# Optimization experiments

Measured on AMD Instinct MI355X. Metric: run time of the kernel, lower is better.

The kernel has to match this reference:

```python
import jax, jax.numpy as jnp
import numpy as np

HEADS = 8
DIM_HEADS = 64
M_DIM = 512
X_DIM = 512
MEM_NUM = 512
N = 16384
PERCENT = 0.25
LAY_NUMBER = 2       # outer refinement iterations
CROSS_LAYERS = 2     # layers inside M_cross_layers
EPS = 1e-5


def setup_inputs() -> dict:
    key = jax.random.key(0)
    ks = jax.random.split(key, 8)
    data = jax.random.normal(ks[0], (N, X_DIM), dtype=jnp.float32)
    Memory = jax.random.normal(ks[1], (MEM_NUM, M_DIM), dtype=jnp.float32)
    # to_kv: Linear(X_dim, 2*kv_dim, bias=False); kv_dim = heads*dim_heads
    Wkv = jax.random.normal(ks[2], (X_DIM, 2 * HEADS * DIM_HEADS), dtype=jnp.float32) * 0.02
    # per cross layer: to_q (no bias) and mutl_heads (with bias)
    Wq = jax.random.normal(ks[3], (CROSS_LAYERS, M_DIM, HEADS * DIM_HEADS), dtype=jnp.float32) * 0.02
    Wm = jax.random.normal(ks[4], (CROSS_LAYERS, HEADS * DIM_HEADS, M_DIM), dtype=jnp.float32) * 0.02
    bm = jnp.zeros((CROSS_LAYERS, M_DIM), dtype=jnp.float32)
    return {"data": data, "Memory": Memory, "Wkv": Wkv, "Wq": Wq, "Wm": Wm, "bm": bm, "istest": 0}


def _layer_norm(x):
    # F.layer_norm over last dim, no affine params
    mu = jnp.mean(x, axis=-1, keepdims=True)
    var = jnp.var(x, axis=-1, keepdims=True)
    return (x - mu) * jax.lax.rsqrt(var + EPS)


def _cross_layer(M, X, Wkv, Wq_l, Wm_l, bm_l):
    # cross_att + residual + layernorm (SublayerConnection); FFN is dead code in source
    q = (M @ Wq_l).reshape(MEM_NUM, HEADS, DIM_HEADS).transpose(1, 0, 2)      # [h, m, dh]
    kv = X @ Wkv                                                              # [n, 2*h*dh]
    k, v = jnp.split(kv, 2, axis=-1)
    k = k.reshape(-1, HEADS, DIM_HEADS).transpose(1, 0, 2)                    # [h, n, dh]
    v = v.reshape(-1, HEADS, DIM_HEADS).transpose(1, 0, 2)
    sim = jnp.einsum('hid,hjd->hij', q, k) * (DIM_HEADS ** -0.5)              # [h, m, n]
    att = jax.nn.softmax(sim, axis=-1)
    o = jnp.einsum('hij,hjd->hid', att, v)                                    # [h, m, dh]
    o = o.transpose(1, 0, 2).reshape(MEM_NUM, HEADS * DIM_HEADS)
    out = o @ Wm_l + bm_l                                                     # [m, M_dim]
    return _layer_norm(out + M)


def _cross_layers(M, X, Wkv, Wq, Wm, bm):
    for l in range(CROSS_LAYERS):
        M = _cross_layer(M, X, Wkv, Wq[l], Wm[l], bm[l])
    return M


def _calucate_sim(data, M):
    # per-sample landmark similarity: max scaled dot product against memory rows
    logits = (data @ M.T) * (DIM_HEADS ** -0.5)   # [N, mem]
    return jnp.max(logits, axis=-1)               # [N]


def _calucate_emb(data, M):
    logits = (data @ M.T) * (DIM_HEADS ** -0.5)   # [N, mem]
    logp = jax.nn.log_softmax(logits, axis=-1)
    p = jnp.exp(logp)
    out_ebs = p @ M                               # soft memory readout [N, M_dim]
    result_loss = -jnp.mean(jnp.max(logp, axis=-1))
    lse = jax.scipy.special.logsumexp(logits, axis=-1)
    zloss = jnp.mean(lse ** 2)                    # router-style z-loss
    return out_ebs, result_loss, zloss


def _select(data, sim_M, k):
    _, top_idx = jax.lax.top_k(sim_M, k)
    X = jnp.zeros_like(data)
    return X.at[top_idx].set(data[top_idx])


def reference(data, Memory, Wkv, Wq, Wm, bm, istest):
    M = Memory
    sim_M = _calucate_sim(data, M)
    percent_count = int(data.shape[0] * PERCENT)
    if not istest:
        X = _select(data, sim_M, percent_count)
        for _ in range(LAY_NUMBER):
            M = _cross_layers(M, X, Wkv, Wq, Wm, bm)
            sim_M = _calucate_sim(data, M)
            X = _select(data, sim_M, percent_count)
    out_ebs, result_loss, zloss = _calucate_emb(data, M)
    return (sim_M, out_ebs, result_loss, zloss)
```

## Files before the change

### kernel.cpp

```cpp
#include <hip/hip_runtime.h>
#include <cstdint>

#define N_DATA 16384
#define DIM 512
#define MEM 512
#define KSEL 4096
#define NH 8
#define DH 64
#define KVDIM 1024
#define SCALE 0.125f
#define ZCNT 12288.0f
#define LN_EPS 1e-5f
#define NSPLIT 4

typedef unsigned short u16;
using short8 = __attribute__((ext_vector_type(8))) short;
using f32x4  = __attribute__((ext_vector_type(4))) float;

__device__ __forceinline__ unsigned fenc(float x) {
    unsigned u = __float_as_uint(x);
    return (u & 0x80000000u) ? ~u : (u | 0x80000000u);
}
__device__ __forceinline__ u16 f2bf(float x) {
    unsigned u = __float_as_uint(x);
    u += 0x7fffu + ((u >> 16) & 1u);
    return (u16)(u >> 16);
}
__device__ __forceinline__ float bf2f(u16 h) { return __uint_as_float(((unsigned)h) << 16); }

__device__ __forceinline__ float waveSum(float v) {
#pragma unroll
    for (int o = 32; o > 0; o >>= 1) v += __shfl_down(v, o, 64);
    return v;
}
__device__ float blockSum(float v) {
    __shared__ float sh[4];
    __syncthreads();
    v = waveSum(v);
    if ((threadIdx.x & 63) == 0) sh[threadIdx.x >> 6] = v;
    __syncthreads();
    if (threadIdx.x == 0) { float s = sh[0]; for (int i = 1; i < 4; ++i) s += sh[i]; sh[0] = s; }
    __syncthreads();
    return sh[0];
}

template<int ROWS, int NW, bool GATHER>
__device__ __forceinline__ void stage_tile(const u16* __restrict__ src, int ld, int k0,
                                           int row0, const int* __restrict__ gidx,
                                           u16* lds, int wave)
{
    constexpr int NI = ROWS / 16;
    const int lane = threadIdx.x & 63;
#pragma unroll
    for (int i = wave; i < NI; i += NW) {
        const int ch = i * 64 + lane;
        const int r = ch >> 2, cc = ch & 3;
        int rg = row0 + r;
        if (GATHER) rg = gidx[rg];
        const u16* g = src + (long)rg * ld + k0 + cc * 8;
        u16* l = lds + i * 512;
        __builtin_amdgcn_global_load_lds((const __attribute__((address_space(1))) void*)g,
                                         (__attribute__((address_space(3))) void*)l,
                                         16, 0, 0);
    }
}

template<int WM, int WN, bool GATHER, int EPI, bool BIAS>
__global__ __launch_bounds__(WM * WN * 64)
void mfma_gemm(const u16* __restrict__ A, const u16* __restrict__ B,
               const float* __restrict__ bias, const int* __restrict__ gidx,
               void* __restrict__ Cv, unsigned* __restrict__ simenc,
               int K, int lda, int ldb, int ldc,
               long zsA, long zsB, long zsC, int zdiv, long zsplitC, float alpha)
{
    constexpr int BM = WM * 64, BN = WN * 64, NW = WM * WN;
    __shared__ __align__(16) u16 As[BM * 32];
    __shared__ __align__(16) u16 Bs[BN * 32];

    const int t = threadIdx.x;
    const int wave = t >> 6, lane = t & 63;
    const int wr = wave / WN, wc = wave % WN;
    const int l15 = lane & 15, l4 = lane >> 4;
    const int bm0 = blockIdx.x * BM, bn0 = blockIdx.y * BN;
    const int zs = (int)blockIdx.z % zdiv;
    const int zh = (int)blockIdx.z / zdiv;
    A += (long)zh * zsA;
    B += (long)zh * zsB;

    f32x4 acc[4][4];
#pragma unroll
    for (int i = 0; i < 4; ++i)
#pragma unroll
        for (int j = 0; j < 4; ++j)
#pragma unroll
            for (int r = 0; r < 4; ++r) acc[i][j][r] = 0.f;

    const int Kd = K / zdiv;
    const int kbeg = zs * Kd;
    for (int k0 = kbeg; k0 < kbeg + Kd; k0 += 32) {
        stage_tile<BM, NW, GATHER>(A, lda, k0, bm0, gidx, As, wave);
        stage_tile<BN, NW, false>(B, ldb, k0, bn0, nullptr, Bs, wave);
        __syncthreads();
        short8 a[4], b[4];
#pragma unroll
        for (int fm = 0; fm < 4; ++fm)
            a[fm] = *(const short8*)(As + (wr * 64 + fm * 16 + l15) * 32 + l4 * 8);
#pragma unroll
        for (int fn = 0; fn < 4; ++fn)
            b[fn] = *(const short8*)(Bs + (wc * 64 + fn * 16 + l15) * 32 + l4 * 8);
#pragma unroll
        for (int fm = 0; fm < 4; ++fm)
#pragma unroll
            for (int fn = 0; fn < 4; ++fn)
                acc[fm][fn] = __builtin_amdgcn_mfma_f32_16x16x32_bf16(a[fm], b[fn], acc[fm][fn], 0, 0, 0);
        __syncthreads();
    }

    if (EPI == 0) {
        float* C = (float*)Cv + (long)zh * zsC + (long)zs * zsplitC;
#pragma unroll
        for (int fm = 0; fm < 4; ++fm)
#pragma unroll
            for (int fn = 0; fn < 4; ++fn)
#pragma unroll
                for (int r = 0; r < 4; ++r) {
                    const int row = bm0 + wr * 64 + fm * 16 + l4 * 4 + r;
                    const int col = bn0 + wc * 64 + fn * 16 + l15;
                    float v = alpha * acc[fm][fn][r];
                    if (BIAS) v += bias[col];
                    C[(long)row * ldc + col] = v;
                }
    } else {
        u16* C = (u16*)Cv + (long)zh * zsC + (long)zs * zsplitC;
#pragma unroll
        for (int fm = 0; fm < 4; ++fm)
#pragma unroll
            for (int fn = 0; fn < 4; ++fn)
#pragma unroll
                for (int r = 0; r < 4; ++r) {
                    const int row = bm0 + wr * 64 + fm * 16 + l4 * 4 + r;
                    const int col = bn0 + wc * 64 + fn * 16 + l15;
                    float v = alpha * acc[fm][fn][r];
                    if (BIAS) v += bias[col];
                    C[(long)row * ldc + col] = f2bf(v);
                }
    }
    (void)simenc;
}

template<int EPI>
__global__ __launch_bounds__(512)
void mfma_gemm_row(const u16* __restrict__ A, const u16* __restrict__ B,
                   const float* __restrict__ bias, const float* __restrict__ Min,
                   unsigned* __restrict__ simenc,
                   float* __restrict__ Mout, u16* __restrict__ Obf,
                   float* __restrict__ simf, float* __restrict__ lse,
                   float* __restrict__ mlp, float alpha)
{
    __shared__ __align__(16) u16 As[64 * 32];
    __shared__ __align__(16) u16 Bs[512 * 32];
    const int t = threadIdx.x, wave = t >> 6, lane = t & 63;
    const int wc = wave;
    const int l15 = lane & 15, l4 = lane >> 4;
    const int bm0 = blockIdx.x * 64;

    f32x4 acc[4][4];
#pragma unroll
    for (int i = 0; i < 4; ++i)
#pragma unroll
        for (int j = 0; j < 4; ++j)
#pragma unroll
            for (int r = 0; r < 4; ++r) acc[i][j][r] = 0.f;

    for (int k0 = 0; k0 < 512; k0 += 32) {
        stage_tile<64, 8, false>(A, 512, k0, bm0, nullptr, As, wave);
        stage_tile<512, 8, false>(B, 512, k0, 0, nullptr, Bs, wave);
        __syncthreads();
        short8 a[4], b[4];
#pragma unroll
        for (int fm = 0; fm < 4; ++fm)
            a[fm] = *(const short8*)(As + (fm * 16 + l15) * 32 + l4 * 8);
#pragma unroll
        for (int fn = 0; fn < 4; ++fn)
            b[fn] = *(const short8*)(Bs + (wc * 64 + fn * 16 + l15) * 32 + l4 * 8);
#pragma unroll
        for (int fm = 0; fm < 4; ++fm)
#pragma unroll
            for (int fn = 0; fn < 4; ++fn)
                acc[fm][fn] = __builtin_amdgcn_mfma_f32_16x16x32_bf16(a[fm], b[fn], acc[fm][fn], 0, 0, 0);
        __syncthreads();
    }

    float* red  = (float*)As;
    float* red2 = red + 512;
    float* rowv = (float*)Bs;

    if (EPI == 0) {
#pragma unroll
        for (int fm = 0; fm < 4; ++fm)
#pragma unroll
            for (int r = 0; r < 4; ++r) {
                float mx = alpha * acc[fm][0][r];
#pragma unroll
                for (int fn = 1; fn < 4; ++fn) mx = fmaxf(mx, alpha * acc[fm][fn][r]);
#pragma unroll
                for (int o = 1; o <= 8; o <<= 1) mx = fmaxf(mx, __shfl_xor(mx, o, 64));
                if (l15 == 0) red[(fm * 16 + l4 * 4 + r) * 8 + wc] = mx;
            }
        __syncthreads();
        if (t < 64) {
            float mx = red[t * 8];
#pragma unroll
            for (int j = 1; j < 8; ++j) mx = fmaxf(mx, red[t * 8 + j]);
            simenc[bm0 + t] = fenc(mx);
        }
    } else if (EPI == 1) {
        float v[4][4][4];
#pragma unroll
        for (int fm = 0; fm < 4; ++fm)
#pragma unroll
            for (int fn = 0; fn < 4; ++fn) {
                const int col = wc * 64 + fn * 16 + l15;
                const float bi = bias[col];
#pragma unroll
                for (int r = 0; r < 4; ++r) {
                    const int row = bm0 + fm * 16 + l4 * 4 + r;
                    v[fm][fn][r] = acc[fm][fn][r] + bi + Min[(long)row * 512 + col];
                }
            }
#pragma unroll
        for (int fm = 0; fm < 4; ++fm)
#pragma unroll
            for (int r = 0; r < 4; ++r) {
                float s = 0.f, s2 = 0.f;
#pragma unroll
                for (int fn = 0; fn < 4; ++fn) { const float x = v[fm][fn][r]; s += x; s2 += x * x; }
#pragma unroll
                for (int o = 1; o <= 8; o <<= 1) { s += __shfl_xor(s, o, 64); s2 += __shfl_xor(s2, o, 64); }
                if (l15 == 0) {
                    red [(fm * 16 + l4 * 4 + r) * 8 + wc] = s;
                    red2[(fm * 16 + l4 * 4 + r) * 8 + wc] = s2;
                }
            }
        __syncthreads();
        if (t < 64) {
            float s = 0.f, s2 = 0.f;
#pragma unroll
            for (int j = 0; j < 8; ++j) { s += red[t * 8 + j]; s2 += red2[t * 8 + j]; }
            const float mu = s * (1.f / 512.f);
            const float var = s2 * (1.f / 512.f) - mu * mu;
            rowv[t] = mu;
            rowv[64 + t] = rsqrtf(var + LN_EPS);
        }
        __syncthreads();
#pragma unroll
        for (int fm = 0; fm < 4; ++fm)
#pragma unroll
            for (int r = 0; r < 4; ++r) {
                const int rl = fm * 16 + l4 * 4 + r;
                const float mu = rowv[rl], rs = rowv[64 + rl];
#pragma unroll
                for (int fn = 0; fn < 4; ++fn) {
                    const int col = wc * 64 + fn * 16 + l15;
                    const float y = (v[fm][fn][r] - mu) * rs;
                    Mout[(long)(bm0 + rl) * 512 + col] = y;
                    Obf [(long)(bm0 + rl) * 512 + col] = f2bf(y);
                }
            }
    } else {
#pragma unroll
        for (int fm = 0; fm < 4; ++fm)
#pragma unroll
            for (int r = 0; r < 4; ++r) {
                float mx = alpha * acc[fm][0][r];
#pragma unroll
                for (int fn = 1; fn < 4; ++fn) mx = fmaxf(mx, alpha * acc[fm][fn][r]);
#pragma unroll
                for (int o = 1; o <= 8; o <<= 1) mx = fmaxf(mx, __shfl_xor(mx, o, 64));
                if (l15 == 0) red[(fm * 16 + l4 * 4 + r) * 8 + wc] = mx;
            }
        __syncthreads();
        if (t < 64) {
            float mx = red[t * 8];
#pragma unroll
            for (int j = 1; j < 8; ++j) mx = fmaxf(mx, red[t * 8 + j]);
            rowv[t] = mx;
        }
        __syncthreads();
#pragma unroll
        for (int fm = 0; fm < 4; ++fm)
#pragma unroll
            for (int r = 0; r < 4; ++r) {
                const int rl = fm * 16 + l4 * 4 + r;
                const float m = rowv[rl];
                float s = 0.f;
#pragma unroll
                for (int fn = 0; fn < 4; ++fn) s += __expf(alpha * acc[fm][fn][r] - m);
#pragma unroll
                for (int o = 1; o <= 8; o <<= 1) s += __shfl_xor(s, o, 64);
                if (l15 == 0) red[rl * 8 + wc] = s;
            }
        __syncthreads();
        if (t < 64) {
            float s = 0.f;
#pragma unroll
            for (int j = 0; j < 8; ++j) s += red[t * 8 + j];
            const float m = rowv[t];
            const float l = m + __logf(s);
            const int gr = bm0 + t;
            simf[gr] = m; lse[gr] = l; mlp[gr] = m - l;
            rowv[64 + t] = l;
        }
        __syncthreads();
#pragma unroll
        for (int fm = 0; fm < 4; ++fm)
#pragma unroll
            for (int r = 0; r < 4; ++r) {
                const int rl = fm * 16 + l4 * 4 + r;
                const float l = rowv[64 + rl];
#pragma unroll
                for (int fn = 0; fn < 4; ++fn) {
                    const int col = wc * 64 + fn * 16 + l15;
                    Obf[(long)(bm0 + rl) * 512 + col] = f2bf(__expf(alpha * acc[fm][fn][r] - l));
                }
            }
    }
}

__global__ __launch_bounds__(256)
void flash_att(const u16* __restrict__ Q, const u16* __restrict__ KV,
               const u16* __restrict__ VT,
               float* __restrict__ oPart, float* __restrict__ mPart,
               float* __restrict__ lPart)
{
    __shared__ __align__(16) u16 Qs[64 * 64];
    __shared__ __align__(16) u16 Ks[2][64 * 64];
    __shared__ __align__(16) u16 Vs[2][64 * 64];
    __shared__ __align__(16) u16 Ps[4][16 * 72];

    const int qt = blockIdx.x, h = blockIdx.y, sp = blockIdx.z;
    const int t = threadIdx.x, wave = t >> 6, lane = t & 63;
    const int l15 = lane & 15, l4 = lane >> 4;

    const u16* Qg = Q + (long)(qt * 64) * 512 + h * 64;
    const u16* Kg = KV + ((long)sp * 1024) * 1024 + h * 64;
    const u16* Vg = VT + ((long)h * 64) * 4096 + sp * 1024;

    auto stageKV = [&](int kt, int buf) {
        const u16* Kt = Kg + (long)(kt * 64) * 1024;
        const u16* Vt = Vg + kt * 64;
#pragma unroll
        for (int i = wave; i < 8; i += 4) {
            const int ch = i * 64 + lane, r = ch >> 3, s = ch & 7;
            __builtin_amdgcn_global_load_lds(
                (const __attribute__((address_space(1))) void*)(Kt + (long)r * 1024 + ((s ^ (r & 7)) * 8)),
                (__attribute__((address_space(3))) void*)(Ks[buf] + i * 512), 16, 0, 0);
        }
#pragma unroll
        for (int i = wave; i < 8; i += 4) {
            const int ch = i * 64 + lane, r = ch >> 3, s = ch & 7;
            __builtin_amdgcn_global_load_lds(
                (const __attribute__((address_space(1))) void*)(Vt + (long)r * 4096 + ((s ^ (r & 7)) * 8)),
                (__attribute__((address_space(3))) void*)(Vs[buf] + i * 512), 16, 0, 0);
        }
    };

#pragma unroll
    for (int i = wave; i < 8; i += 4) {
        const int ch = i * 64 + lane, r = ch >> 3, s = ch & 7;
        __builtin_amdgcn_global_load_lds(
            (const __attribute__((address_space(1))) void*)(Qg + (long)r * 512 + ((s ^ (r & 7)) * 8)),
            (__attribute__((address_space(3))) void*)(Qs + i * 512), 16, 0, 0);
    }
    stageKV(0, 0);
    __syncthreads();

    const int qr = wave * 16 + l15;
    short8 qf0 = *(const short8*)(Qs + qr * 64 + ((0 * 4 + l4) ^ (qr & 7)) * 8);
    short8 qf1 = *(const short8*)(Qs + qr * 64 + ((1 * 4 + l4) ^ (qr & 7)) * 8);

    float m = -3.0e38f, lsum = 0.f;
    f32x4 acc_o[4];
#pragma unroll
    for (int nf = 0; nf < 4; ++nf)
#pragma unroll
        for (int r = 0; r < 4; ++r) acc_o[nf][r] = 0.f;

    u16* myP = &Ps[wave][0];
    constexpr int NT = KSEL / 64 / NSPLIT;
    int cur = 0;

    for (int kt = 0; kt < NT; ++kt) {
        if (kt + 1 < NT) stageKV(kt + 1, cur ^ 1);
        const u16* Kc = Ks[cur];
        const u16* Vc = Vs[cur];
        f32x4 acc_s[4];
#pragma unroll
        for (int mf = 0; mf < 4; ++mf) {
#pragma unroll
            for (int r = 0; r < 4; ++r) acc_s[mf][r] = 0.f;
            const int kr = mf * 16 + l15;
            const short8 ka0 = *(const short8*)(Kc + kr * 64 + ((0 * 4 + l4) ^ (kr & 7)) * 8);
            const short8 ka1 = *(const short8*)(Kc + kr * 64 + ((1 * 4 + l4) ^ (kr & 7)) * 8);
            acc_s[mf] = __builtin_amdgcn_mfma_f32_16x16x32_bf16(ka0, qf0, acc_s[mf], 0, 0, 0);
            acc_s[mf] = __builtin_amdgcn_mfma_f32_16x16x32_bf16(ka1, qf1, acc_s[mf], 0, 0, 0);
        }
        float sv[16];
#pragma unroll
        for (int mf = 0; mf < 4; ++mf)
#pragma unroll
            for (int r = 0; r < 4; ++r) sv[mf * 4 + r] = SCALE * acc_s[mf][r];
        float pm = sv[0];
#pragma unroll
        for (int j = 1; j < 16; ++j) pm = fmaxf(pm, sv[j]);
        pm = fmaxf(pm, __shfl_xor(pm, 16, 64));
        pm = fmaxf(pm, __shfl_xor(pm, 32, 64));
        const float mnew = fmaxf(m, pm);
        const float corr = __expf(m - mnew);
        float rs = 0.f;
#pragma unroll
        for (int j = 0; j < 16; ++j) { sv[j] = __expf(sv[j] - mnew); rs += sv[j]; }
        rs += __shfl_xor(rs, 16, 64);
        rs += __shfl_xor(rs, 32, 64);
        lsum = lsum * corr + rs;
        m = mnew;
        const float cf0 = __shfl(corr, l4 * 4 + 0, 64);
        const float cf1 = __shfl(corr, l4 * 4 + 1, 64);
        const float cf2 = __shfl(corr, l4 * 4 + 2, 64);
        const float cf3 = __shfl(corr, l4 * 4 + 3, 64);
#pragma unroll
        for (int nf = 0; nf < 4; ++nf) {
            acc_o[nf][0] *= cf0; acc_o[nf][1] *= cf1;
            acc_o[nf][2] *= cf2; acc_o[nf][3] *= cf3;
        }
#pragma unroll
        for (int mf = 0; mf < 4; ++mf) {
            ushort4 pw;
            pw.x = f2bf(sv[mf * 4 + 0]); pw.y = f2bf(sv[mf * 4 + 1]);
            pw.z = f2bf(sv[mf * 4 + 2]); pw.w = f2bf(sv[mf * 4 + 3]);
            *(ushort4*)(myP + l15 * 72 + mf * 16 + l4 * 4) = pw;
        }
#pragma unroll
        for (int ks = 0; ks < 2; ++ks) {
            const short8 pa = *(const short8*)(myP + l15 * 72 + ks * 32 + l4 * 8);
#pragma unroll
            for (int nf = 0; nf < 4; ++nf) {
                const int dr = nf * 16 + l15;
                const short8 vb = *(const short8*)(Vc + dr * 64 + ((ks * 4 + l4) ^ (dr & 7)) * 8);
                acc_o[nf] = __builtin_amdgcn_mfma_f32_16x16x32_bf16(pa, vb, acc_o[nf], 0, 0, 0);
            }
        }
        __syncthreads();
        cur ^= 1;
    }

    float* ob = oPart + (((long)sp * NH + h) * 8 + qt) * 4096;
#pragma unroll
    for (int nf = 0; nf < 4; ++nf)
#pragma unroll
        for (int r = 0; r < 4; ++r)
            ob[(wave * 16 + l4 * 4 + r) * 64 + nf * 16 + l15] = acc_o[nf][r];
    if (lane < 16) {
        const int qi = wave * 16 + lane;
        mPart[((sp * NH + h) * 8 + qt) * 64 + qi] = m;
        lPart[((sp * NH + h) * 8 + qt) * 64 + qi] = lsum;
    }
}

__global__ __launch_bounds__(256)
void flash_combine(const float* __restrict__ oPart, const float* __restrict__ mPart,
                   const float* __restrict__ lPart, u16* __restrict__ o_bf)
{
    const int qt = blockIdx.x & 7, h = blockIdx.x >> 3;
    const int t = threadIdx.x;
    const int q = t >> 2, d0 = (t & 3) << 4;
    float mi[NSPLIT], li[NSPLIT];
#pragma unroll
    for (int sp = 0; sp < NSPLIT; ++sp) {
        const int sb = ((sp * NH + h) * 8 + qt) * 64 + q;
        mi[sp] = mPart[sb];
        li[sp] = lPart[sb];
    }
    float ms = 0.f;
#pragma unroll
    for (int sp = 0; sp < NSPLIT; ++sp) ms = fmaxf(ms, mi[sp]);
    float denom = ZCNT * __expf(-ms);
    float f[NSPLIT];
#pragma unroll
    for (int sp = 0; sp < NSPLIT; ++sp) { f[sp] = __expf(mi[sp] - ms); denom += li[sp] * f[sp]; }
    const float inv = 1.f / denom;
    float o[16];
#pragma unroll
    for (int j = 0; j < 16; ++j) o[j] = 0.f;
#pragma unroll
    for (int sp = 0; sp < NSPLIT; ++sp) {
        const float* ob = oPart + (((long)sp * NH + h) * 8 + qt) * 4096 + q * 64 + d0;
        const float fs = f[sp] * inv;
#pragma unroll
        for (int j = 0; j < 16; j += 4) {
            const float4 v = *(const float4*)(ob + j);
            o[j] += fs * v.x; o[j + 1] += fs * v.y; o[j + 2] += fs * v.z; o[j + 3] += fs * v.w;
        }
    }
    u16* op = o_bf + (qt * 64 + q) * 512 + h * 64 + d0;
#pragma unroll
    for (int j = 0; j < 16; j += 4) {
        ushort4 w4;
        w4.x = f2bf(o[j]); w4.y = f2bf(o[j + 1]); w4.z = f2bf(o[j + 2]); w4.w = f2bf(o[j + 3]);
        *(ushort4*)(op + j) = w4;
    }
}

__global__ __launch_bounds__(256)
void conv_f32_bf(const float* __restrict__ s, u16* __restrict__ d, int n)
{
    const int i = (blockIdx.x * 256 + threadIdx.x) * 4;
    if (i >= n) return;
    const float4 v = *(const float4*)(s + i);
    ushort4 o;
    o.x = f2bf(v.x); o.y = f2bf(v.y); o.z = f2bf(v.z); o.w = f2bf(v.w);
    *(ushort4*)(d + i) = o;
}

template<bool INBF>
__global__ __launch_bounds__(256)
void transpose_bf(const void* __restrict__ Sv, u16* __restrict__ D,
                  int Rr, int Cc, int ldS)
{
    __shared__ float tile[32][33];
    const int c0 = blockIdx.x * 32, r0 = blockIdx.y * 32;
    const int tx = threadIdx.x & 31, ty = threadIdx.x >> 5;
#pragma unroll
    for (int j = 0; j < 32; j += 8) {
        const int r = r0 + ty + j, c = c0 + tx;
        float v = INBF ? bf2f(((const u16*)Sv)[(long)r * ldS + c])
                       : ((const float*)Sv)[(long)r * ldS + c];
        tile[ty + j][tx] = v;
    }
    __syncthreads();
#pragma unroll
    for (int j = 0; j < 32; j += 8) {
        const int cO = c0 + ty + j, rO = r0 + tx;
        D[(long)cO * Rr + rO] = f2bf(tile[tx][ty + j]);
    }
}

__global__ __launch_bounds__(256)
void transpose_w4(const float* __restrict__ Wq, const float* __restrict__ Wm,
                  u16* __restrict__ WqT, u16* __restrict__ WmT)
{
    const int z = blockIdx.z;
    const float* S = (z < 2) ? (Wq + (long)z * DIM * DIM) : (Wm + (long)(z - 2) * DIM * DIM);
    u16* D = (z < 2) ? (WqT + (long)z * DIM * DIM) : (WmT + (long)(z - 2) * DIM * DIM);
    __shared__ float tile[32][33];
    const int c0 = blockIdx.x * 32, r0 = blockIdx.y * 32;
    const int tx = threadIdx.x & 31, ty = threadIdx.x >> 5;
#pragma unroll
    for (int j = 0; j < 32; j += 8)
        tile[ty + j][tx] = S[(long)(r0 + ty + j) * DIM + c0 + tx];
    __syncthreads();
#pragma unroll
    for (int j = 0; j < 32; j += 8)
        D[(long)(c0 + ty + j) * DIM + r0 + tx] = f2bf(tile[tx][ty + j]);
}

__device__ __forceinline__ unsigned scan1024_excl(unsigned v, unsigned* wsum)
{
    const int lane = threadIdx.x & 63, wv = threadIdx.x >> 6;
    __syncthreads();
    unsigned x = v;
#pragma unroll
    for (int o = 1; o < 64; o <<= 1) {
        unsigned y = __shfl_up(x, o, 64);
        if (lane >= o) x += y;
    }
    if (lane == 63) wsum[wv] = x;
    __syncthreads();
    if (threadIdx.x < 16) {
        unsigned w2 = wsum[threadIdx.x];
#pragma unroll
        for (int o = 1; o < 16; o <<= 1) {
            unsigned y = __shfl_up(w2, o, 64);
            if ((int)threadIdx.x >= o) w2 += y;
        }
        wsum[threadIdx.x] = w2;
    }
    __syncthreads();
    const unsigned off = (wv > 0) ? wsum[wv - 1] : 0u;
    return off + x - v;
}

#define SEL_T 1024
#define SEL_CH (N_DATA / SEL_T)
__global__ __launch_bounds__(SEL_T)
void select_topk(const unsigned* __restrict__ key, int* __restrict__ idxo, int k)
{
    __shared__ unsigned whist[16][256];
    __shared__ unsigned hist[256];
    __shared__ unsigned wsum[16];
    __shared__ unsigned sh_bin, sh_r;
    const int t = threadIdx.x;
    const int wv = t >> 6;
    const int base = t * SEL_CH;

    unsigned kreg[SEL_CH];
#pragma unroll
    for (int c = 0; c < SEL_CH; ++c) kreg[c] = key[base + c];

    unsigned prefix = 0, mask = 0;
    unsigned r = (unsigned)k;
    for (int p = 3; p >= 0; --p) {
        __syncthreads();
        for (int i = t; i < 16 * 256; i += SEL_T) ((unsigned*)whist)[i] = 0u;
        __syncthreads();
#pragma unroll
        for (int c = 0; c < SEL_CH; ++c) {
            const unsigned kv = kreg[c];
            if ((kv & mask) == prefix)
                atomicAdd(&whist[wv][(kv >> (p * 8)) & 255u], 1u);
        }
        __syncthreads();
        if (t < 256) {
            unsigned s = 0;
#pragma unroll
            for (int wq = 0; wq < 16; ++wq) s += whist[wq][t];
            hist[t] = s;
        }
        __syncthreads();
        if (t < 64) {
            const int b0 = 255 - 4 * t;
            const unsigned c = hist[b0] + hist[b0 - 1] + hist[b0 - 2] + hist[b0 - 3];
            unsigned x = c;
#pragma unroll
            for (int o = 1; o < 64; o <<= 1) {
                unsigned y = __shfl_up(x, o, 64);
                if (t >= o) x += y;
            }
            const unsigned pre = x - c;
            if (pre < r && r <= x) {
                unsigned cum = pre;
#pragma unroll
                for (int j = 0; j < 4; ++j) {
                    const int b = b0 - j;
                    cum += hist[b];
                    if (cum >= r) { sh_bin = (unsigned)b; sh_r = r - (cum - hist[b]); break; }
                }
            }
        }
        __syncthreads();
        prefix |= sh_bin << (p * 8);
        mask |= 255u << (p * 8);
        r = sh_r;
    }
    const unsigned thr = prefix;
    const unsigned ties = r;

    unsigned ceq = 0;
#pragma unroll
    for (int c = 0; c < SEL_CH; ++c) ceq += (kreg[c] == thr) ? 1u : 0u;
    const unsigned eqbase = scan1024_excl(ceq, wsum);
    unsigned eq = eqbase, csel = 0;
#pragma unroll
    for (int c = 0; c < SEL_CH; ++c) {
        const unsigned kv = kreg[c];
        bool s;
        if (kv == thr) { s = (eq < ties); ++eq; }
        else s = (kv > thr);
        csel += s ? 1u : 0u;
    }
    unsigned pos = scan1024_excl(csel, wsum);
    eq = eqbase;
#pragma unroll
    for (int c = 0; c < SEL_CH; ++c) {
        const unsigned kv = kreg[c];
        bool s;
        if (kv == thr) { s = (eq < ties); ++eq; }
        else s = (kv > thr);
        if (s) idxo[pos++] = base + c;
    }
}

__global__ __launch_bounds__(256)
void reduce_loss(const float* __restrict__ lse, const float* __restrict__ mlp,
                 float* __restrict__ o2)
{
    const int t = threadIdx.x;
    float s1 = 0.f, s2 = 0.f;
    for (int i = t; i < N_DATA; i += 256) { s1 += mlp[i]; float l = lse[i]; s2 += l * l; }
    s1 = blockSum(s1);
    s2 = blockSum(s2);
    if (t == 0) { o2[0] = -s1 * (1.f / N_DATA); o2[1] = s2 * (1.f / N_DATA); }
}

extern "C" void kernel_launch(void* const* d_in, const int* in_sizes, int n_in,
                              void* d_out, int out_size, void* d_ws, size_t ws_size,
                              hipStream_t stream)
{
    (void)in_sizes; (void)n_in; (void)out_size; (void)ws_size;
    const float* data   = (const float*)d_in[0];
    const float* Memory = (const float*)d_in[1];
    const float* Wkv    = (const float*)d_in[2];
    const float* Wq     = (const float*)d_in[3];
    const float* Wm     = (const float*)d_in[4];
    const float* bm     = (const float*)d_in[5];
    float* out = (float*)d_out;

    char* w = (char*)d_ws;
    unsigned* simenc = (unsigned*)(w + 0);
    int*   idx     = (int*)  (w + 65536);
    float* lse     = (float*)(w + 81920);
    float* mlp     = (float*)(w + 147456);
    float* Ma      = (float*)(w + 262144);
    float* Mb      = (float*)(w + 1310720);
    u16*   Mbf0    = (u16*)  (w + 2359296);
    u16*   MT_bf   = (u16*)  (w + 2883584);
    u16*   WqT_bf  = (u16*)  (w + 3407872);
    u16*   WmT_bf  = (u16*)  (w + 4456448);
    u16*   WkvT_bf = (u16*)  (w + 5505024);
    u16*   q_bf    = (u16*)  (w + 6553600);
    u16*   o_bf    = (u16*)  (w + 7077888);
    u16*   data_bf = (u16*)  (w + 8650752);
    u16*   kvsel_bf= (u16*)  (w + 25427968);
    u16*   vT_bf   = (u16*)  (w + 33816576);
    float* oPart   = (float*)(w + 38010880);
    float* mPart   = (float*)(w + 42205184);
    float* lPart   = (float*)(w + 42270720);
    u16*   logits_bf = (u16*)(w + 54788096);
    u16*   Mbfa    = (u16*)  (w + 88342528);
    u16*   Mbfb    = (u16*)  (w + 88866816);

    conv_f32_bf<<<(N_DATA * DIM / 4 + 255) / 256, 256, 0, stream>>>(data, data_bf, N_DATA * DIM);
    conv_f32_bf<<<(DIM * DIM / 4 + 255) / 256, 256, 0, stream>>>(Memory, Mbf0, DIM * DIM);
    transpose_bf<false><<<dim3(KVDIM / 32, DIM / 32), 256, 0, stream>>>(Wkv, WkvT_bf, DIM, KVDIM, KVDIM);
    transpose_w4<<<dim3(16, 16, 4), 256, 0, stream>>>(Wq, Wm, WqT_bf, WmT_bf);

    auto sim_select_kv = [&](const u16* Mrows_bf) {
        mfma_gemm_row<0><<<N_DATA / 64, 512, 0, stream>>>(
            data_bf, Mrows_bf, nullptr, nullptr, simenc,
            nullptr, nullptr, nullptr, nullptr, nullptr, SCALE);
        select_topk<<<1, SEL_T, 0, stream>>>(simenc, idx, KSEL);
        mfma_gemm<2, 2, true, 1, false><<<dim3(32, 8, 1), 256, 0, stream>>>(
            data_bf, WkvT_bf, nullptr, idx, kvsel_bf, nullptr,
            DIM, DIM, DIM, KVDIM, 0, 0, 0, 1, 0, 1.0f);
        transpose_bf<true><<<dim3(DIM / 32, KSEL / 32), 256, 0, stream>>>(
            kvsel_bf + DIM, vT_bf, KSEL, DIM, KVDIM);
    };

    auto cross = [&](const float* Mcur, const u16* Mcur_bf, float* Mnext, u16* Mnext_bf, int l) {
        mfma_gemm<2, 2, false, 1, false><<<dim3(4, 4, 1), 256, 0, stream>>>(
            Mcur_bf, WqT_bf + (long)l * DIM * DIM, nullptr, nullptr, q_bf, nullptr,
            DIM, DIM, DIM, DIM, 0, 0, 0, 1, 0, 1.0f);
        flash_att<<<dim3(8, NH, NSPLIT), 256, 0, stream>>>(q_bf, kvsel_bf, vT_bf, oPart, mPart, lPart);
        flash_combine<<<64, 256, 0, stream>>>(oPart, mPart, lPart, o_bf);
        mfma_gemm_row<1><<<DIM / 64, 512, 0, stream>>>(
            o_bf, WmT_bf + (long)l * DIM * DIM, bm + (long)l * DIM, Mcur, nullptr,
            Mnext, Mnext_bf, nullptr, nullptr, nullptr, 1.0f);
    };

    const float* Mcur = Memory;
    const u16*  curbf = Mbf0;
    float* Mnext = Ma;
    u16*   nextbf = Mbfa;
    sim_select_kv(curbf);
    for (int it = 0; it < 2; ++it) {
        for (int l = 0; l < 2; ++l) {
            cross(Mcur, curbf, Mnext, nextbf, l);
            Mcur = Mnext; curbf = nextbf;
            Mnext = (Mcur == Ma) ? Mb : Ma;
            nextbf = (curbf == Mbfa) ? Mbfb : Mbfa;
        }
        if (it == 0) sim_select_kv(curbf);
    }

    mfma_gemm_row<2><<<N_DATA / 64, 512, 0, stream>>>(
        data_bf, curbf, nullptr, nullptr, nullptr,
        nullptr, logits_bf, out, lse, mlp, SCALE);
    transpose_bf<false><<<dim3(16, 16), 256, 0, stream>>>(Mcur, MT_bf, MEM, DIM, DIM);
    mfma_gemm<2, 2, false, 0, false><<<dim3(128, 4, 1), 256, 0, stream>>>(
        logits_bf, MT_bf, nullptr, nullptr, out + N_DATA, nullptr,
        MEM, MEM, MEM, DIM, 0, 0, 0, 1, 0, 1.0f);
    reduce_loss<<<1, 256, 0, stream>>>(lse, mlp, out + N_DATA + (long)N_DATA * DIM);
}
```

Measured before the change: 445.5 us.

## Fuse Q projection into flash attention, split LN epilogue, atomic row-max sim

The Q projection GEMM is folded into the flash attention kernel: each block computes its 64x64 Q tile directly from M and WqT using MFMA reading global memory, which removes a launch and the q_bf round trip. The row-wide output-projection+LayerNorm kernel (only 8 blocks) is replaced by a 16-block tiled GEMM with bias followed by a separate add+LayerNorm kernel. The similarity row-max now runs on the 2D tiled GEMM with atomicMax into a zeroed buffer instead of full-row blocks. In exchange, each flash block recomputes Q for its head (redundantly across the 4 splits), and the change adds a memset and extra launches.

```diff
diff --git a/kernel.cpp b/kernel.cpp
--- a/kernel.cpp
+++ b/kernel.cpp
@@ -116,7 +116,22 @@
         __syncthreads();
     }
 
-    if (EPI == 0) {
+    if (EPI == 2) {
+#pragma unroll
+        for (int fm = 0; fm < 4; ++fm)
+#pragma unroll
+            for (int r = 0; r < 4; ++r) {
+                float mx = acc[fm][0][r];
+#pragma unroll
+                for (int fn = 1; fn < 4; ++fn) mx = fmaxf(mx, acc[fm][fn][r]);
+#pragma unroll
+                for (int o = 8; o >= 1; o >>= 1) mx = fmaxf(mx, __shfl_xor(mx, o, 64));
+                if (l15 == 0) {
+                    const int row = bm0 + wr * 64 + fm * 16 + l4 * 4 + r;
+                    atomicMax(simenc + row, fenc(alpha * mx));
+                }
+            }
+    } else if (EPI == 0) {
         float* C = (float*)Cv + (long)zh * zsC + (long)zs * zsplitC;
 #pragma unroll
         for (int fm = 0; fm < 4; ++fm)
@@ -145,17 +160,12 @@
                     C[(long)row * ldc + col] = f2bf(v);
                 }
     }
-    (void)simenc;
-}
-
-template<int EPI>
+}
+
 __global__ __launch_bounds__(512)
-void mfma_gemm_row(const u16* __restrict__ A, const u16* __restrict__ B,
-                   const float* __restrict__ bias, const float* __restrict__ Min,
-                   unsigned* __restrict__ simenc,
-                   float* __restrict__ Mout, u16* __restrict__ Obf,
-                   float* __restrict__ simf, float* __restrict__ lse,
-                   float* __restrict__ mlp, float alpha)
+void mfma_gemm_sm(const u16* __restrict__ A, const u16* __restrict__ B,
+                  u16* __restrict__ Obf, float* __restrict__ simf,
+                  float* __restrict__ lse, float* __restrict__ mlp, float alpha)
 {
     __shared__ __align__(16) u16 As[64 * 32];
     __shared__ __align__(16) u16 Bs[512 * 32];
@@ -192,144 +202,69 @@
     }
 
     float* red  = (float*)As;
-    float* red2 = red + 512;
     float* rowv = (float*)Bs;
 
-    if (EPI == 0) {
-#pragma unroll
-        for (int fm = 0; fm < 4; ++fm)
-#pragma unroll
-            for (int r = 0; r < 4; ++r) {
-                float mx = alpha * acc[fm][0][r];
-#pragma unroll
-                for (int fn = 1; fn < 4; ++fn) mx = fmaxf(mx, alpha * acc[fm][fn][r]);
-#pragma unroll
-                for (int o = 1; o <= 8; o <<= 1) mx = fmaxf(mx, __shfl_xor(mx, o, 64));
-                if (l15 == 0) red[(fm * 16 + l4 * 4 + r) * 8 + wc] = mx;
-            }
-        __syncthreads();
-        if (t < 64) {
-            float mx = red[t * 8];
-#pragma unroll
-            for (int j = 1; j < 8; ++j) mx = fmaxf(mx, red[t * 8 + j]);
-            simenc[bm0 + t] = fenc(mx);
-        }
-    } else if (EPI == 1) {
-        float v[4][4][4];
-#pragma unroll
-        for (int fm = 0; fm < 4; ++fm)
+#pragma unroll
+    for (int fm = 0; fm < 4; ++fm)
+#pragma unroll
+        for (int r = 0; r < 4; ++r) {
+            float mx = alpha * acc[fm][0][r];
+#pragma unroll
+            for (int fn = 1; fn < 4; ++fn) mx = fmaxf(mx, alpha * acc[fm][fn][r]);
+#pragma unroll
+            for (int o = 1; o <= 8; o <<= 1) mx = fmaxf(mx, __shfl_xor(mx, o, 64));
+            if (l15 == 0) red[(fm * 16 + l4 * 4 + r) * 8 + wc] = mx;
+        }
+    __syncthreads();
+    if (t < 64) {
+        float mx = red[t * 8];
+#pragma unroll
+        for (int j = 1; j < 8; ++j) mx = fmaxf(mx, red[t * 8 + j]);
+        rowv[t] = mx;
+    }
+    __syncthreads();
+#pragma unroll
+    for (int fm = 0; fm < 4; ++fm)
+#pragma unroll
+        for (int r = 0; r < 4; ++r) {
+            const int rl = fm * 16 + l4 * 4 + r;
+            const float m = rowv[rl];
+            float s = 0.f;
+#pragma unroll
+            for (int fn = 0; fn < 4; ++fn) s += __expf(alpha * acc[fm][fn][r] - m);
+#pragma unroll
+            for (int o = 1; o <= 8; o <<= 1) s += __shfl_xor(s, o, 64);
+            if (l15 == 0) red[rl * 8 + wc] = s;
+        }
+    __syncthreads();
+    if (t < 64) {
+        float s = 0.f;
+#pragma unroll
+        for (int j = 0; j < 8; ++j) s += red[t * 8 + j];
+        const float m = rowv[t];
+        const float l = m + __logf(s);
+        const int gr = bm0 + t;
+        simf[gr] = m; lse[gr] = l; mlp[gr] = m - l;
+        rowv[64 + t] = l;
+    }
+    __syncthreads();
+#pragma unroll
+    for (int fm = 0; fm < 4; ++fm)
+#pragma unroll
+        for (int r = 0; r < 4; ++r) {
+            const int rl = fm * 16 + l4 * 4 + r;
+            const float l = rowv[64 + rl];
 #pragma unroll
             for (int fn = 0; fn < 4; ++fn) {
                 const int col = wc * 64 + fn * 16 + l15;
-                const float bi = bias[col];
-#pragma unroll
-                for (int r = 0; r < 4; ++r) {
-                    const int row = bm0 + fm * 16 + l4 * 4 + r;
-                    v[fm][fn][r] = acc[fm][fn][r] + bi + Min[(long)row * 512 + col];
-                }
+                Obf[(long)(bm0 + rl) * 512 + col] = f2bf(__expf(alpha * acc[fm][fn][r] - l));
             }
-#pragma unroll
-        for (int fm = 0; fm < 4; ++fm)
-#pragma unroll
-            for (int r = 0; r < 4; ++r) {
-                float s = 0.f, s2 = 0.f;
-#pragma unroll
-                for (int fn = 0; fn < 4; ++fn) { const float x = v[fm][fn][r]; s += x; s2 += x * x; }
-#pragma unroll
-                for (int o = 1; o <= 8; o <<= 1) { s += __shfl_xor(s, o, 64); s2 += __shfl_xor(s2, o, 64); }
-                if (l15 == 0) {
-                    red [(fm * 16 + l4 * 4 + r) * 8 + wc] = s;
-                    red2[(fm * 16 + l4 * 4 + r) * 8 + wc] = s2;
-                }
-            }
-        __syncthreads();
-        if (t < 64) {
-            float s = 0.f, s2 = 0.f;
-#pragma unroll
-            for (int j = 0; j < 8; ++j) { s += red[t * 8 + j]; s2 += red2[t * 8 + j]; }
-            const float mu = s * (1.f / 512.f);
-            const float var = s2 * (1.f / 512.f) - mu * mu;
-            rowv[t] = mu;
-            rowv[64 + t] = rsqrtf(var + LN_EPS);
-        }
-        __syncthreads();
-#pragma unroll
-        for (int fm = 0; fm < 4; ++fm)
-#pragma unroll
-            for (int r = 0; r < 4; ++r) {
-                const int rl = fm * 16 + l4 * 4 + r;
-                const float mu = rowv[rl], rs = rowv[64 + rl];
-#pragma unroll
-                for (int fn = 0; fn < 4; ++fn) {
-                    const int col = wc * 64 + fn * 16 + l15;
-                    const float y = (v[fm][fn][r] - mu) * rs;
-                    Mout[(long)(bm0 + rl) * 512 + col] = y;
-                    Obf [(long)(bm0 + rl) * 512 + col] = f2bf(y);
-                }
-            }
-    } else {
-#pragma unroll
-        for (int fm = 0; fm < 4; ++fm)
-#pragma unroll
-            for (int r = 0; r < 4; ++r) {
-                float mx = alpha * acc[fm][0][r];
-#pragma unroll
-                for (int fn = 1; fn < 4; ++fn) mx = fmaxf(mx, alpha * acc[fm][fn][r]);
-#pragma unroll
-                for (int o = 1; o <= 8; o <<= 1) mx = fmaxf(mx, __shfl_xor(mx, o, 64));
-                if (l15 == 0) red[(fm * 16 + l4 * 4 + r) * 8 + wc] = mx;
-            }
-        __syncthreads();
-        if (t < 64) {
-            float mx = red[t * 8];
-#pragma unroll
-            for (int j = 1; j < 8; ++j) mx = fmaxf(mx, red[t * 8 + j]);
-            rowv[t] = mx;
-        }
-        __syncthreads();
-#pragma unroll
-        for (int fm = 0; fm < 4; ++fm)
-#pragma unroll
-            for (int r = 0; r < 4; ++r) {
-                const int rl = fm * 16 + l4 * 4 + r;
-                const float m = rowv[rl];
-                float s = 0.f;
-#pragma unroll
-                for (int fn = 0; fn < 4; ++fn) s += __expf(alpha * acc[fm][fn][r] - m);
-#pragma unroll
-                for (int o = 1; o <= 8; o <<= 1) s += __shfl_xor(s, o, 64);
-                if (l15 == 0) red[rl * 8 + wc] = s;
-            }
-        __syncthreads();
-        if (t < 64) {
-            float s = 0.f;
-#pragma unroll
-            for (int j = 0; j < 8; ++j) s += red[t * 8 + j];
-            const float m = rowv[t];
-            const float l = m + __logf(s);
-            const int gr = bm0 + t;
-            simf[gr] = m; lse[gr] = l; mlp[gr] = m - l;
-            rowv[64 + t] = l;
-        }
-        __syncthreads();
-#pragma unroll
-        for (int fm = 0; fm < 4; ++fm)
-#pragma unroll
-            for (int r = 0; r < 4; ++r) {
-                const int rl = fm * 16 + l4 * 4 + r;
-                const float l = rowv[64 + rl];
-#pragma unroll
-                for (int fn = 0; fn < 4; ++fn) {
-                    const int col = wc * 64 + fn * 16 + l15;
-                    Obf[(long)(bm0 + rl) * 512 + col] = f2bf(__expf(alpha * acc[fm][fn][r] - l));
-                }
-            }
-    }
+        }
 }
 
 __global__ __launch_bounds__(256)
-void flash_att(const u16* __restrict__ Q, const u16* __restrict__ KV,
-               const u16* __restrict__ VT,
+void flash_att(const u16* __restrict__ Mbf, const u16* __restrict__ WqT,
+               const u16* __restrict__ KV, const u16* __restrict__ VT,
                float* __restrict__ oPart, float* __restrict__ mPart,
                float* __restrict__ lPart)
 {
@@ -342,7 +277,6 @@
     const int t = threadIdx.x, wave = t >> 6, lane = t & 63;
     const int l15 = lane & 15, l4 = lane >> 4;
 
-    const u16* Qg = Q + (long)(qt * 64) * 512 + h * 64;
     const u16* Kg = KV + ((long)sp * 1024) * 1024 + h * 64;
     const u16* Vg = VT + ((long)h * 64) * 4096 + sp * 1024;
 
@@ -365,14 +299,34 @@
         }
     };
 
-#pragma unroll
-    for (int i = wave; i < 8; i += 4) {
-        const int ch = i * 64 + lane, r = ch >> 3, s = ch & 7;
-        __builtin_amdgcn_global_load_lds(
-            (const __attribute__((address_space(1))) void*)(Qg + (long)r * 512 + ((s ^ (r & 7)) * 8)),
-            (__attribute__((address_space(3))) void*)(Qs + i * 512), 16, 0, 0);
-    }
     stageKV(0, 0);
+
+    f32x4 accq[4];
+#pragma unroll
+    for (int fn = 0; fn < 4; ++fn)
+#pragma unroll
+        for (int r = 0; r < 4; ++r) accq[fn][r] = 0.f;
+    {
+        const u16* Ag = Mbf + (long)(qt * 64 + wave * 16 + l15) * 512 + l4 * 8;
+        const u16* Bg = WqT + (long)(h * 64 + l15) * 512 + l4 * 8;
+#pragma unroll 4
+        for (int k0 = 0; k0 < 512; k0 += 32) {
+            const short8 a = *(const short8*)(Ag + k0);
+#pragma unroll
+            for (int fn = 0; fn < 4; ++fn) {
+                const short8 b = *(const short8*)(Bg + (long)fn * 16 * 512 + k0);
+                accq[fn] = __builtin_amdgcn_mfma_f32_16x16x32_bf16(a, b, accq[fn], 0, 0, 0);
+            }
+        }
+    }
+#pragma unroll
+    for (int fn = 0; fn < 4; ++fn)
+#pragma unroll
+        for (int r = 0; r < 4; ++r) {
+            const int qrow = wave * 16 + l4 * 4 + r;
+            const int col = fn * 16 + l15;
+            Qs[qrow * 64 + (((col >> 3) ^ (qrow & 7)) << 3) + (col & 7)] = f2bf(accq[fn][r]);
+        }
     __syncthreads();
 
     const int qr = wave * 16 + l15;
@@ -678,6 +632,26 @@
         else s = (kv > thr);
         if (s) idxo[pos++] = base + c;
     }
+}
+
+__global__ __launch_bounds__(256)
+void ln_add_k(const float* __restrict__ outp, const float* __restrict__ Min,
+              float* __restrict__ Mout, u16* __restrict__ Mbf)
+{
+    const int r = blockIdx.x;
+    const int t = threadIdx.x;
+    float x0 = outp[r * DIM + t] + Min[r * DIM + t];
+    float x1 = outp[r * DIM + t + 256] + Min[r * DIM + t + 256];
+    float s = blockSum(x0 + x1);
+    float s2 = blockSum(x0 * x0 + x1 * x1);
+    const float mu = s * (1.f / DIM);
+    const float var = s2 * (1.f / DIM) - mu * mu;
+    const float rs = rsqrtf(var + LN_EPS);
+    const float y0 = (x0 - mu) * rs, y1 = (x1 - mu) * rs;
+    Mout[r * DIM + t] = y0;
+    Mout[r * DIM + t + 256] = y1;
+    Mbf[r * DIM + t] = f2bf(y0);
+    Mbf[r * DIM + t + 256] = f2bf(y1);
 }
 
 __global__ __launch_bounds__(256)
@@ -717,8 +691,8 @@
     u16*   WqT_bf  = (u16*)  (w + 3407872);
     u16*   WmT_bf  = (u16*)  (w + 4456448);
     u16*   WkvT_bf = (u16*)  (w + 5505024);
-    u16*   q_bf    = (u16*)  (w + 6553600);
     u16*   o_bf    = (u16*)  (w + 7077888);
+    float* outp    = (float*)(w + 7602176);
     u16*   data_bf = (u16*)  (w + 8650752);
     u16*   kvsel_bf= (u16*)  (w + 25427968);
     u16*   vT_bf   = (u16*)  (w + 33816576);
@@ -735,9 +709,10 @@
     transpose_w4<<<dim3(16, 16, 4), 256, 0, stream>>>(Wq, Wm, WqT_bf, WmT_bf);
 
     auto sim_select_kv = [&](const u16* Mrows_bf) {
-        mfma_gemm_row<0><<<N_DATA / 64, 512, 0, stream>>>(
-            data_bf, Mrows_bf, nullptr, nullptr, simenc,
-            nullptr, nullptr, nullptr, nullptr, nullptr, SCALE);
+        hipMemsetAsync(simenc, 0, N_DATA * 4, stream);
+        mfma_gemm<2, 2, false, 2, false><<<dim3(128, 4, 1), 256, 0, stream>>>(
+            data_bf, Mrows_bf, nullptr, nullptr, nullptr, simenc,
+            DIM, DIM, DIM, 0, 0, 0, 0, 1, 0, SCALE);
         select_topk<<<1, SEL_T, 0, stream>>>(simenc, idx, KSEL);
         mfma_gemm<2, 2, true, 1, false><<<dim3(32, 8, 1), 256, 0, stream>>>(
             data_bf, WkvT_bf, nullptr, idx, kvsel_bf, nullptr,
@@ -747,14 +722,13 @@
     };
 
     auto cross = [&](const float* Mcur, const u16* Mcur_bf, float* Mnext, u16* Mnext_bf, int l) {
-        mfma_gemm<2, 2, false, 1, false><<<dim3(4, 4, 1), 256, 0, stream>>>(
-            Mcur_bf, WqT_bf + (long)l * DIM * DIM, nullptr, nullptr, q_bf, nullptr,
+        flash_att<<<dim3(8, NH, NSPLIT), 256, 0, stream>>>(
+            Mcur_bf, WqT_bf + (long)l * DIM * DIM, kvsel_bf, vT_bf, oPart, mPart, lPart);
+        flash_combine<<<64, 256, 0, stream>>>(oPart, mPart, lPart, o_bf);
+        mfma_gemm<2, 2, false, 0, true><<<dim3(4, 4, 1), 256, 0, stream>>>(
+            o_bf, WmT_bf + (long)l * DIM * DIM, bm + (long)l * DIM, nullptr, outp, nullptr,
             DIM, DIM, DIM, DIM, 0, 0, 0, 1, 0, 1.0f);
-        flash_att<<<dim3(8, NH, NSPLIT), 256, 0, stream>>>(q_bf, kvsel_bf, vT_bf, oPart, mPart, lPart);
-        flash_combine<<<64, 256, 0, stream>>>(oPart, mPart, lPart, o_bf);
-        mfma_gemm_row<1><<<DIM / 64, 512, 0, stream>>>(
-            o_bf, WmT_bf + (long)l * DIM * DIM, bm + (long)l * DIM, Mcur, nullptr,
-            Mnext, Mnext_bf, nullptr, nullptr, nullptr, 1.0f);
+        ln_add_k<<<DIM, 256, 0, stream>>>(outp, Mcur, Mnext, Mnext_bf);
     };
 
     const float* Mcur = Memory;
@@ -772,9 +746,8 @@
         if (it == 0) sim_select_kv(curbf);
     }
 
-    mfma_gemm_row<2><<<N_DATA / 64, 512, 0, stream>>>(
-        data_bf, curbf, nullptr, nullptr, nullptr,
-        nullptr, logits_bf, out, lse, mlp, SCALE);
+    mfma_gemm_sm<<<N_DATA / 64, 512, 0, stream>>>(
+        data_bf, curbf, logits_bf, out, lse, mlp, SCALE);
     transpose_bf<false><<<dim3(16, 16), 256, 0, stream>>>(Mcur, MT_bf, MEM, DIM, DIM);
     mfma_gemm<2, 2, false, 0, false><<<dim3(128, 4, 1), 256, 0, stream>>>(
         logits_bf, MT_bf, nullptr, nullptr, out + N_DATA, nullptr,
```

Result: faster. 389.7 us (-12.5%).
